# Kernel tuning notes

Hardware: AMD Instinct MI355X
Metric: run time of the kernel (lower is better)

The kernel has to match this reference:

```python
import jax, jax.numpy as jnp
import numpy as np

P, B, A, NT = 2, 96, 32, 24
N = B * A
MD, MA, MW = 4, 4, 2
NPOLB = MD + MA
C_LK = 0.089793561062583294  # 1 / (2 * pi**1.5)


def _norm(v):
    return v / jnp.sqrt(jnp.sum(v * v, -1, keepdims=True) + 1e-12)


def _gat_atoms(c, i):
    # c: [P,B,A,3], i: [P,B,K] -> [P,B,K,3]
    return jnp.take_along_axis(c, jnp.broadcast_to(i[..., None], i.shape + (3,)), axis=2)


def setup_inputs():
    key = jax.random.key(0)
    rng = np.random.default_rng(0)
    inp = {}
    inp["pose_coords"] = jax.random.normal(key, (P, N, 3), jnp.float32) * 8.0
    inp["pose_stack_block_type"] = jnp.asarray(rng.integers(0, NT, (P, B)), jnp.int32)
    inp["pose_stack_min_bond_separation"] = jnp.full((P, B, B), 6, jnp.int32)
    inp["bt_n_atoms"] = jnp.full((NT,), A, jnp.int32)
    bonds = np.stack([np.arange(A), (np.arange(A) + 1) % A], -1)
    inp["bt_all_bonds"] = jnp.asarray(np.broadcast_to(bonds, (NT, A, 2)).copy(), jnp.int32)
    rngs = np.stack([np.arange(A), np.arange(A) + 1], -1)
    inp["bt_atom_all_bond_ranges"] = jnp.asarray(np.broadcast_to(rngs, (NT, A, 2)).copy(), jnp.int32)
    inp["bt_tile_n_donH"] = jnp.asarray(rng.integers(1, MD + 1, (NT,)), jnp.int32)
    inp["bt_tile_n_acc"] = jnp.asarray(rng.integers(1, MA + 1, (NT,)), jnp.int32)
    donH = np.broadcast_to(2 * np.arange(MD) + 1, (NT, MD)).copy()
    inp["bt_tile_donH_inds"] = jnp.asarray(donH, jnp.int32)
    inp["bt_tile_don_hvy_inds"] = jnp.asarray(donH - 1, jnp.int32)
    inp["bt_tile_acc_inds"] = jnp.asarray(np.broadcast_to(8 + np.arange(MA), (NT, MA)).copy(), jnp.int32)
    inp["bt_tile_hybridization"] = jnp.asarray(rng.integers(0, 3, (NT, MA)), jnp.int32)
    is_h = np.zeros((NT, A), np.int32)
    is_h[:, 1:8:2] = 1
    inp["bt_atom_is_hydrogen"] = jnp.asarray(is_h)
    par = np.empty((NT, A, 4), np.float32)
    par[..., 0] = rng.uniform(1.4, 2.2, (NT, A))   # lj_radius
    par[..., 1] = rng.uniform(-6.0, 6.0, (NT, A))  # lk_dgfree
    par[..., 2] = rng.uniform(3.0, 3.6, (NT, A))   # lk_lambda
    par[..., 3] = rng.uniform(3.0, 15.0, (NT, A))  # lk_volume
    inp["bt_tile_lk_ball_params"] = jnp.asarray(par)
    pd = np.minimum(np.abs(np.arange(A)[:, None] - np.arange(A)[None, :]), 6)
    inp["bt_path_distance"] = jnp.asarray(np.broadcast_to(pd, (NT, A, A)).copy(), jnp.int32)
    inp["lk_ball_global_params"] = jnp.asarray([6.0, 3.709, 2.828], jnp.float32)   # cutoff, ramp_width_A2, d2_low
    inp["water_gen_global_params"] = jnp.asarray([2.65, 2.0943951], jnp.float32)   # water dist, water bond angle
    inp["sp2_water_tors"] = jnp.asarray([0.0, np.pi], jnp.float32)
    inp["sp3_water_tors"] = jnp.asarray([np.pi / 3.0, -np.pi / 3.0], jnp.float32)
    inp["ring_water_tors"] = jnp.asarray([0.0, np.pi / 2.0], jnp.float32)
    return inp


def reference(pose_coords, pose_stack_block_type, pose_stack_min_bond_separation,
              bt_n_atoms, bt_all_bonds, bt_atom_all_bond_ranges,
              bt_tile_n_donH, bt_tile_n_acc, bt_tile_donH_inds, bt_tile_don_hvy_inds,
              bt_tile_acc_inds, bt_tile_hybridization, bt_atom_is_hydrogen,
              bt_tile_lk_ball_params, bt_path_distance,
              lk_ball_global_params, water_gen_global_params,
              sp2_water_tors, sp3_water_tors, ring_water_tors):
    bt = pose_stack_block_type
    coords = pose_coords.reshape(P, B, A, 3)
    wdist = water_gen_global_params[0]
    wang = water_gen_global_params[1]
    # ---- step 1a: donor waters placed along heavy->H direction ----
    hvy_i = bt_tile_don_hvy_inds[bt]
    H_i = bt_tile_donH_inds[bt]                                              # [P,B,MD]
    hvy = _gat_atoms(coords, hvy_i)
    Hxyz = _gat_atoms(coords, H_i)
    don_w = hvy + wdist * _norm(Hxyz - hvy)                                  # [P,B,MD,3]
    don_mask = jnp.arange(MD) < bt_tile_n_donH[bt][..., None]                # [P,B,MD]
    don_w = jnp.broadcast_to(don_w[..., None, :], (P, B, MD, MW, 3))
    don_wm = don_mask[..., None] & (jnp.arange(MW) == 0)                     # one water per donH
    # ---- step 1b: acceptor waters via hybridization-dependent torsion (NeRF) ----
    acc_i = bt_tile_acc_inds[bt]                                             # [P,B,MA]
    ranges0 = bt_atom_all_bond_ranges[bt][..., 0]                            # [P,B,A]
    bonds1 = bt_all_bonds[bt][..., 1]                                        # [P,B,A]
    base_i = jnp.take_along_axis(bonds1, jnp.take_along_axis(ranges0, acc_i, axis=2), axis=2)
    base2_i = jnp.take_along_axis(bonds1, jnp.take_along_axis(ranges0, base_i, axis=2), axis=2)
    cxyz = _gat_atoms(coords, acc_i)
    bxyz = _gat_atoms(coords, base_i)
    axyz = _gat_atoms(coords, base2_i)
    e1 = _norm(cxyz - bxyz)
    nrm = _norm(jnp.cross(bxyz - axyz, e1))
    e2 = jnp.cross(nrm, e1)
    tors_tab = jnp.stack([sp2_water_tors, sp3_water_tors, ring_water_tors])  # [3,MW]
    chi = tors_tab[bt_tile_hybridization[bt]]                                # [P,B,MA,MW]
    ct, st = jnp.cos(wang), jnp.sin(wang)
    acc_w = (cxyz[..., None, :]
             + (-wdist * ct) * e1[..., None, :]
             + (wdist * st) * jnp.cos(chi)[..., None] * e2[..., None, :]
             + (wdist * st) * jnp.sin(chi)[..., None] * nrm[..., None, :])   # [P,B,MA,MW,3]
    acc_mask = jnp.arange(MA) < bt_tile_n_acc[bt][..., None]
    acc_wm = jnp.broadcast_to(acc_mask[..., None], (P, B, MA, MW))
    # ---- assemble polar sites + waters ----
    waters = jnp.concatenate([don_w, acc_w], axis=2).reshape(P, B * NPOLB, MW, 3)
    wmask = jnp.concatenate([don_wm, acc_wm], axis=2).reshape(P, B * NPOLB, MW)
    pol_loc = jnp.concatenate([hvy_i, acc_i], axis=2)                        # [P,B,NPOLB]
    pol_mask = jnp.concatenate([don_mask, acc_mask], axis=2).reshape(P, B * NPOLB)
    gidx = (jnp.arange(B)[None, :, None] * A + pol_loc).reshape(P, B * NPOLB)
    # ---- gather per-atom data ----
    params_flat = bt_tile_lk_ball_params[bt].reshape(P, N, 4)
    heavy = bt_atom_is_hydrogen[bt].reshape(P, N) == 0
    xp = jnp.take_along_axis(pose_coords, jnp.broadcast_to(gidx[..., None], gidx.shape + (3,)), axis=1)
    pp = jnp.take_along_axis(params_flat, jnp.broadcast_to(gidx[..., None], gidx.shape + (4,)), axis=1)
    # ---- step 2: pair distances + bond-separation mask ----
    diff = xp[:, :, None, :] - pose_coords[:, None, :, :]                    # [P,NPOL,N,3]
    d2 = jnp.maximum(jnp.sum(diff * diff, -1), 1e-2)
    d = jnp.sqrt(d2)
    b_i = gidx // A
    a_i = gidx % A
    b_j = jnp.arange(N) // A
    a_j = jnp.arange(N) % A
    bti = jnp.take_along_axis(bt, b_i, axis=1)
    intra = bt_path_distance[bti[:, :, None], a_i[:, :, None], a_j[None, None, :]]
    inter = pose_stack_min_bond_separation[jnp.arange(P)[:, None, None], b_i[:, :, None], b_j[None, None, :]]
    sep = jnp.where(b_i[:, :, None] == b_j[None, None, :], intra, inter)
    cutoff = lk_ball_global_params[0]
    ramp2 = lk_ball_global_params[1]
    d2_low = lk_ball_global_params[2]
    mask = (sep >= 4) & heavy[:, None, :] & pol_mask[:, :, None] & (d < cutoff)
    # ---- isotropic LK desolvation of polar atom i by occluder j ----
    ri, dgi, lami = pp[..., 0], pp[..., 1], pp[..., 2]
    rj, volj = params_flat[..., 0], params_flat[..., 3]
    x = (d - (ri[:, :, None] + rj[:, None, :])) / lami[:, :, None]
    lk_iso = C_LK * dgi[:, :, None] * volj[:, None, :] / lami[:, :, None] * jnp.exp(-x * x) / d2
    lk_iso = jnp.where(mask, lk_iso, 0.0)
    # ---- lk-ball fraction from water-site occlusion ----
    wdiff = waters[:, :, :, None, :] - pose_coords[:, None, None, :, :]      # [P,NPOL,MW,N,3]
    d2w = jnp.sum(wdiff * wdiff, -1)
    d2w = jnp.where(wmask[..., None], d2w, 1e9)
    d2wmin = jnp.min(d2w, axis=2)                                            # [P,NPOL,N]
    wt = jnp.clip((d2_low + ramp2 - d2wmin) / ramp2, 0.0, 1.0)
    frac = wt * wt * (3.0 - 2.0 * wt)
    return jnp.stack([jnp.sum(lk_iso, (1, 2)), jnp.sum(lk_iso * frac, (1, 2))])  # [2,P]
```

## Files before the change

### kernel.cpp

```cpp
#include <hip/hip_runtime.h>
#include <math.h>

constexpr int P  = 2;
constexpr int B  = 96;
constexpr int A  = 32;
constexpr int N  = B * A;
constexpr int MD = 4;
constexpr int MA = 4;
constexpr int NPOL = MD + MA;
constexpr int SJ = 2;
constexpr int JS = N / SJ;
constexpr int JPT = JS / 256;
constexpr float C_LK = 0.0897935610625833f;

__global__ void zero_out_kernel(float* out) {
    int t = threadIdx.x;
    if (t < 2 * P) out[t] = 0.0f;
}

__global__ __launch_bounds__(256) void lkball_kernel(
    const float* __restrict__ pose_coords,
    const int*   __restrict__ block_type,
    const int*   __restrict__ min_sep,
    const int*   __restrict__ all_bonds,
    const int*   __restrict__ bond_ranges,
    const int*   __restrict__ n_donH,
    const int*   __restrict__ n_acc,
    const int*   __restrict__ donH_inds,
    const int*   __restrict__ don_hvy_inds,
    const int*   __restrict__ acc_inds,
    const int*   __restrict__ hyb,
    const int*   __restrict__ is_h,
    const float* __restrict__ lk_params,
    const int*   __restrict__ path_dist,
    const float* __restrict__ glob,
    const float* __restrict__ wglob,
    const float* __restrict__ sp2t,
    const float* __restrict__ sp3t,
    const float* __restrict__ ringt,
    float*       __restrict__ out)
{
    __shared__ float spolar[NPOL][16];
    __shared__ int   spolai[NPOL];
    __shared__ int   s_bt[B];
    __shared__ int   smsep[B];
    __shared__ int   spath[NPOL * A];
    __shared__ float red0[4], red1[4];

    const int bid   = blockIdx.x;
    const int p     = bid / (B * SJ);
    const int rem   = bid % (B * SJ);
    const int b     = rem / SJ;
    const int slice = rem % SJ;
    const int tid   = threadIdx.x;

    if (tid < NPOL) {
        const int k  = tid;
        const int bt = block_type[p * B + b];
        const float wdist = wglob[0];
        const float wang  = wglob[1];
        float xp[3], w0[3], w1[3];
        int   a_i, valid;
        if (k < MD) {
            valid = (k < n_donH[bt]) ? 1 : 0;
            const int hvy = don_hvy_inds[bt * MD + k];
            const int Hi  = donH_inds[bt * MD + k];
            a_i = hvy;
            const float* hc = pose_coords + (size_t)(p * N + b * A + hvy) * 3;
            const float* Hc = pose_coords + (size_t)(p * N + b * A + Hi) * 3;
            float dx = Hc[0] - hc[0], dy = Hc[1] - hc[1], dz = Hc[2] - hc[2];
            float inv = 1.0f / sqrtf(dx * dx + dy * dy + dz * dz + 1e-12f);
            xp[0] = hc[0]; xp[1] = hc[1]; xp[2] = hc[2];
            w0[0] = hc[0] + wdist * dx * inv;
            w0[1] = hc[1] + wdist * dy * inv;
            w0[2] = hc[2] + wdist * dz * inv;
            w1[0] = hc[0] + 1.0e3f; w1[1] = hc[1] + 1.0e3f; w1[2] = hc[2] + 1.0e3f;
        } else {
            const int kk = k - MD;
            valid = (kk < n_acc[bt]) ? 1 : 0;
            const int ai = acc_inds[bt * MA + kk];
            a_i = ai;
            const int r0    = bond_ranges[(bt * A + ai) * 2 + 0];
            const int base  = all_bonds[(bt * A + r0) * 2 + 1];
            const int r0b   = bond_ranges[(bt * A + base) * 2 + 0];
            const int base2 = all_bonds[(bt * A + r0b) * 2 + 1];
            const float* c  = pose_coords + (size_t)(p * N + b * A + ai)    * 3;
            const float* bx = pose_coords + (size_t)(p * N + b * A + base)  * 3;
            const float* ax = pose_coords + (size_t)(p * N + b * A + base2) * 3;

            float e1x = c[0] - bx[0], e1y = c[1] - bx[1], e1z = c[2] - bx[2];
            float inv1 = 1.0f / sqrtf(e1x * e1x + e1y * e1y + e1z * e1z + 1e-12f);
            e1x *= inv1; e1y *= inv1; e1z *= inv1;

            float ux = bx[0] - ax[0], uy = bx[1] - ax[1], uz = bx[2] - ax[2];
            float nx = uy * e1z - uz * e1y;
            float ny = uz * e1x - ux * e1z;
            float nz = ux * e1y - uy * e1x;
            float inv2 = 1.0f / sqrtf(nx * nx + ny * ny + nz * nz + 1e-12f);
            nx *= inv2; ny *= inv2; nz *= inv2;
            float e2x = ny * e1z - nz * e1y;
            float e2y = nz * e1x - nx * e1z;
            float e2z = nx * e1y - ny * e1x;

            const int hy = hyb[bt * MA + kk];
            const float* tab = (hy == 0) ? sp2t : ((hy == 1) ? sp3t : ringt);
            const float ct = cosf(wang), st = sinf(wang);
            float c0 = cosf(tab[0]), s0 = sinf(tab[0]);
            float c1 = cosf(tab[1]), s1 = sinf(tab[1]);

            xp[0] = c[0]; xp[1] = c[1]; xp[2] = c[2];
            w0[0] = c[0] - wdist * ct * e1x + wdist * st * c0 * e2x + wdist * st * s0 * nx;
            w0[1] = c[1] - wdist * ct * e1y + wdist * st * c0 * e2y + wdist * st * s0 * ny;
            w0[2] = c[2] - wdist * ct * e1z + wdist * st * c0 * e2z + wdist * st * s0 * nz;
            w1[0] = c[0] - wdist * ct * e1x + wdist * st * c1 * e2x + wdist * st * s1 * nx;
            w1[1] = c[1] - wdist * ct * e1y + wdist * st * c1 * e2y + wdist * st * s1 * ny;
            w1[2] = c[2] - wdist * ct * e1z + wdist * st * c1 * e2z + wdist * st * s1 * nz;
        }
        const float* pr = lk_params + (size_t)(bt * A + a_i) * 4;
        const float lam = pr[2];
        spolar[k][0] = xp[0]; spolar[k][1] = xp[1]; spolar[k][2] = xp[2];
        spolar[k][3] = w0[0]; spolar[k][4] = w0[1]; spolar[k][5] = w0[2];
        spolar[k][6] = w1[0]; spolar[k][7] = w1[1]; spolar[k][8] = w1[2];
        spolar[k][9]  = pr[0];
        spolar[k][10] = valid ? (C_LK * pr[1] / lam) : 0.0f;
        spolar[k][11] = 1.0f / lam;
        spolai[k] = a_i;
    }
    if (tid >= 64 && tid < 64 + B)   s_bt[tid - 64]   = block_type[p * B + (tid - 64)];
    if (tid >= 160 && tid < 160 + B) smsep[tid - 160] = min_sep[(p * B + b) * B + (tid - 160)];
    __syncthreads();

    {
        const int k  = tid >> 5;
        const int aj = tid & 31;
        const int bt = s_bt[b];
        spath[tid] = path_dist[(bt * A + spolai[k]) * A + aj];
    }
    __syncthreads();

    const float cutoff = glob[0];
    const float inv_ramp2 = 1.0f / glob[1];
    const float c3 = glob[2] + glob[1];
    const int a_j = tid & 31;
    const int jbase = slice * JS + tid;

    float cx[JPT], cy[JPT], cz[JPT], rj[JPT], ve[JPT];
    float msep_f[JPT];
    int   intra[JPT];
#pragma unroll
    for (int i = 0; i < JPT; ++i) {
        const int j   = jbase + 256 * i;
        const int b_j = j >> 5;
        const float* cj = pose_coords + (size_t)(p * N + j) * 3;
        cx[i] = cj[0]; cy[i] = cj[1]; cz[i] = cj[2];
        const int bt_j = s_bt[b_j];
        const int hv   = is_h[bt_j * A + a_j];
        const float4 pj = *(const float4*)(lk_params + (size_t)(bt_j * A + a_j) * 4);
        rj[i] = pj.x;
        ve[i] = hv ? 0.0f : pj.w;
        msep_f[i] = (float)smsep[b_j];
        intra[i]  = (b_j == b);
    }

    float acc0 = 0.0f, acc1 = 0.0f;

#pragma unroll
    for (int k = 0; k < NPOL; ++k) {
        const float px = spolar[k][0], py = spolar[k][1], pz = spolar[k][2];
        const float w0x = spolar[k][3], w0y = spolar[k][4], w0z = spolar[k][5];
        const float w1x = spolar[k][6], w1y = spolar[k][7], w1z = spolar[k][8];
        const float ri = spolar[k][9], pref = spolar[k][10], inv_lam = spolar[k][11];
        const float path_k = (float)spath[k * A + a_j];

#pragma unroll
        for (int i = 0; i < JPT; ++i) {
            const float dx = px - cx[i], dy = py - cy[i], dz = pz - cz[i];
            float d2 = fmaf(dx, dx, fmaf(dy, dy, dz * dz));
            d2 = fmaxf(d2, 0.01f);
            const float d = __builtin_amdgcn_sqrtf(d2);
            const float sep = intra[i] ? path_k : msep_f[i];
            const bool ok = (sep >= 4.0f) & (d < cutoff);

            const float x = (d - ri - rj[i]) * inv_lam;
            float lk = pref * ve[i] * __expf(-x * x) * __builtin_amdgcn_rcpf(d2);
            lk = ok ? lk : 0.0f;

            const float d0x = w0x - cx[i], d0y = w0y - cy[i], d0z = w0z - cz[i];
            const float d1x = w1x - cx[i], d1y = w1y - cy[i], d1z = w1z - cz[i];
            const float d2w0 = fmaf(d0x, d0x, fmaf(d0y, d0y, d0z * d0z));
            const float d2w1 = fmaf(d1x, d1x, fmaf(d1y, d1y, d1z * d1z));
            const float d2wmin = fminf(d2w0, d2w1);
            float wt = (c3 - d2wmin) * inv_ramp2;
            wt = fminf(fmaxf(wt, 0.0f), 1.0f);
            const float frac = wt * wt * (3.0f - 2.0f * wt);

            acc0 += lk;
            acc1 = fmaf(lk, frac, acc1);
        }
    }

    for (int off = 32; off > 0; off >>= 1) {
        acc0 += __shfl_down(acc0, off);
        acc1 += __shfl_down(acc1, off);
    }
    const int wave = tid >> 6;
    const int lane = tid & 63;
    if (lane == 0) { red0[wave] = acc0; red1[wave] = acc1; }
    __syncthreads();
    if (tid == 0) {
        atomicAdd(&out[p],     red0[0] + red0[1] + red0[2] + red0[3]);
        atomicAdd(&out[P + p], red1[0] + red1[1] + red1[2] + red1[3]);
    }
}

extern "C" void kernel_launch(void* const* d_in, const int* in_sizes, int n_in,
                              void* d_out, int out_size, void* d_ws, size_t ws_size,
                              hipStream_t stream) {
    const float* pose_coords  = (const float*)d_in[0];
    const int*   block_type   = (const int*)  d_in[1];
    const int*   min_sep      = (const int*)  d_in[2];
    const int*   all_bonds    = (const int*)  d_in[4];
    const int*   bond_ranges  = (const int*)  d_in[5];
    const int*   n_donH       = (const int*)  d_in[6];
    const int*   n_acc        = (const int*)  d_in[7];
    const int*   donH_inds    = (const int*)  d_in[8];
    const int*   don_hvy_inds = (const int*)  d_in[9];
    const int*   acc_inds     = (const int*)  d_in[10];
    const int*   hyb          = (const int*)  d_in[11];
    const int*   is_h         = (const int*)  d_in[12];
    const float* lk_params    = (const float*)d_in[13];
    const int*   path_dist    = (const int*)  d_in[14];
    const float* glob         = (const float*)d_in[15];
    const float* wglob        = (const float*)d_in[16];
    const float* sp2t         = (const float*)d_in[17];
    const float* sp3t         = (const float*)d_in[18];
    const float* ringt        = (const float*)d_in[19];
    float* out = (float*)d_out;

    zero_out_kernel<<<1, 64, 0, stream>>>(out);

    const int nblocks = P * B * SJ;
    lkball_kernel<<<nblocks, 256, 0, stream>>>(
        pose_coords, block_type, min_sep, all_bonds, bond_ranges,
        n_donH, n_acc, donH_inds, don_hvy_inds, acc_inds, hyb, is_h,
        lk_params, path_dist, glob, wglob, sp2t, sp3t, ringt, out);
}
```

Measured before the change: 113.1 us.

## Precompute polar-atom water sites in a prep kernel and split occluders finer

```diff
diff --git a/kernel.cpp b/kernel.cpp
--- a/kernel.cpp
+++ b/kernel.cpp
@@ -8,20 +8,17 @@
 constexpr int MD = 4;
 constexpr int MA = 4;
 constexpr int NPOL = MD + MA;
-constexpr int SJ = 2;
+constexpr int SJ = 4;
 constexpr int JS = N / SJ;
 constexpr int JPT = JS / 256;
-constexpr float C_LK = 0.0897935610625833f;
-
-__global__ void zero_out_kernel(float* out) {
-    int t = threadIdx.x;
-    if (t < 2 * P) out[t] = 0.0f;
-}
-
-__global__ __launch_bounds__(256) void lkball_kernel(
+constexpr int NPTOT = P * B * NPOL;
+constexpr float C_LK  = 0.0897935610625833f;
+constexpr float LOG2E = 1.4426950408889634f;
+
+
+__global__ __launch_bounds__(256) void prep_kernel(
     const float* __restrict__ pose_coords,
     const int*   __restrict__ block_type,
-    const int*   __restrict__ min_sep,
     const int*   __restrict__ all_bonds,
     const int*   __restrict__ bond_ranges,
     const int*   __restrict__ n_donH,
@@ -30,18 +27,108 @@
     const int*   __restrict__ don_hvy_inds,
     const int*   __restrict__ acc_inds,
     const int*   __restrict__ hyb,
+    const float* __restrict__ lk_params,
+    const float* __restrict__ wglob,
+    const float* __restrict__ sp2t,
+    const float* __restrict__ sp3t,
+    const float* __restrict__ ringt,
+    float*       __restrict__ ws,
+    float*       __restrict__ out)
+{
+    const int t = blockIdx.x * 256 + threadIdx.x;
+    if (t < 2 * P) out[t] = 0.0f;
+    if (t >= NPTOT) return;
+
+    const int p = t / (B * NPOL);
+    const int r = t % (B * NPOL);
+    const int b = r / NPOL;
+    const int k = r % NPOL;
+    const int bt = block_type[p * B + b];
+    const float wdist = wglob[0];
+    const float wang  = wglob[1];
+
+    float xp[3], w0[3], w1[3];
+    int a_i, valid;
+    if (k < MD) {
+        valid = (k < n_donH[bt]) ? 1 : 0;
+        const int hvy = don_hvy_inds[bt * MD + k];
+        const int Hi  = donH_inds[bt * MD + k];
+        a_i = hvy;
+        const float* hc = pose_coords + (size_t)(p * N + b * A + hvy) * 3;
+        const float* Hc = pose_coords + (size_t)(p * N + b * A + Hi) * 3;
+        float dx = Hc[0] - hc[0], dy = Hc[1] - hc[1], dz = Hc[2] - hc[2];
+        float inv = 1.0f / sqrtf(dx * dx + dy * dy + dz * dz + 1e-12f);
+        xp[0] = hc[0]; xp[1] = hc[1]; xp[2] = hc[2];
+        w0[0] = hc[0] + wdist * dx * inv;
+        w0[1] = hc[1] + wdist * dy * inv;
+        w0[2] = hc[2] + wdist * dz * inv;
+        w1[0] = hc[0] + 1.0e3f; w1[1] = hc[1] + 1.0e3f; w1[2] = hc[2] + 1.0e3f;
+    } else {
+        const int kk = k - MD;
+        valid = (kk < n_acc[bt]) ? 1 : 0;
+        const int ai = acc_inds[bt * MA + kk];
+        a_i = ai;
+        const int r0    = bond_ranges[(bt * A + ai) * 2 + 0];
+        const int base  = all_bonds[(bt * A + r0) * 2 + 1];
+        const int r0b   = bond_ranges[(bt * A + base) * 2 + 0];
+        const int base2 = all_bonds[(bt * A + r0b) * 2 + 1];
+        const float* c  = pose_coords + (size_t)(p * N + b * A + ai)    * 3;
+        const float* bx = pose_coords + (size_t)(p * N + b * A + base)  * 3;
+        const float* ax = pose_coords + (size_t)(p * N + b * A + base2) * 3;
+
+        float e1x = c[0] - bx[0], e1y = c[1] - bx[1], e1z = c[2] - bx[2];
+        float inv1 = 1.0f / sqrtf(e1x * e1x + e1y * e1y + e1z * e1z + 1e-12f);
+        e1x *= inv1; e1y *= inv1; e1z *= inv1;
+
+        float ux = bx[0] - ax[0], uy = bx[1] - ax[1], uz = bx[2] - ax[2];
+        float nx = uy * e1z - uz * e1y;
+        float ny = uz * e1x - ux * e1z;
+        float nz = ux * e1y - uy * e1x;
+        float inv2 = 1.0f / sqrtf(nx * nx + ny * ny + nz * nz + 1e-12f);
+        nx *= inv2; ny *= inv2; nz *= inv2;
+        float e2x = ny * e1z - nz * e1y;
+        float e2y = nz * e1x - nx * e1z;
+        float e2z = nx * e1y - ny * e1x;
+
+        const int hy = hyb[bt * MA + kk];
+        const float* tab = (hy == 0) ? sp2t : ((hy == 1) ? sp3t : ringt);
+        const float ct = cosf(wang), st = sinf(wang);
+        float c0 = cosf(tab[0]), s0 = sinf(tab[0]);
+        float c1 = cosf(tab[1]), s1 = sinf(tab[1]);
+
+        xp[0] = c[0]; xp[1] = c[1]; xp[2] = c[2];
+        w0[0] = c[0] - wdist * ct * e1x + wdist * st * c0 * e2x + wdist * st * s0 * nx;
+        w0[1] = c[1] - wdist * ct * e1y + wdist * st * c0 * e2y + wdist * st * s0 * ny;
+        w0[2] = c[2] - wdist * ct * e1z + wdist * st * c0 * e2z + wdist * st * s0 * nz;
+        w1[0] = c[0] - wdist * ct * e1x + wdist * st * c1 * e2x + wdist * st * s1 * nx;
+        w1[1] = c[1] - wdist * ct * e1y + wdist * st * c1 * e2y + wdist * st * s1 * ny;
+        w1[2] = c[2] - wdist * ct * e1z + wdist * st * c1 * e2z + wdist * st * s1 * nz;
+    }
+    const float* pr = lk_params + (size_t)(bt * A + a_i) * 4;
+    const float lam = pr[2];
+    float* dst = ws + (size_t)t * 16;
+    dst[0]  = xp[0]; dst[1] = xp[1]; dst[2] = xp[2];
+    dst[3]  = w0[0]; dst[4] = w0[1]; dst[5] = w0[2];
+    dst[6]  = w1[0]; dst[7] = w1[1]; dst[8] = w1[2];
+    dst[9]  = pr[0];
+    dst[10] = valid ? (C_LK * pr[1] / lam) : 0.0f;
+    dst[11] = -LOG2E / (lam * lam);
+    dst[12] = __int_as_float(a_i);
+    dst[13] = 0.0f; dst[14] = 0.0f; dst[15] = 0.0f;
+}
+
+__global__ __launch_bounds__(256, 3) void lkball_kernel(
+    const float* __restrict__ pose_coords,
+    const int*   __restrict__ block_type,
+    const int*   __restrict__ min_sep,
     const int*   __restrict__ is_h,
     const float* __restrict__ lk_params,
     const int*   __restrict__ path_dist,
     const float* __restrict__ glob,
-    const float* __restrict__ wglob,
-    const float* __restrict__ sp2t,
-    const float* __restrict__ sp3t,
-    const float* __restrict__ ringt,
+    const float* __restrict__ ws,
     float*       __restrict__ out)
 {
     __shared__ float spolar[NPOL][16];
-    __shared__ int   spolai[NPOL];
     __shared__ int   s_bt[B];
     __shared__ int   smsep[B];
     __shared__ int   spath[NPOL * A];
@@ -54,77 +141,9 @@
     const int slice = rem % SJ;
     const int tid   = threadIdx.x;
 
-    if (tid < NPOL) {
-        const int k  = tid;
-        const int bt = block_type[p * B + b];
-        const float wdist = wglob[0];
-        const float wang  = wglob[1];
-        float xp[3], w0[3], w1[3];
-        int   a_i, valid;
-        if (k < MD) {
-            valid = (k < n_donH[bt]) ? 1 : 0;
-            const int hvy = don_hvy_inds[bt * MD + k];
-            const int Hi  = donH_inds[bt * MD + k];
-            a_i = hvy;
-            const float* hc = pose_coords + (size_t)(p * N + b * A + hvy) * 3;
-            const float* Hc = pose_coords + (size_t)(p * N + b * A + Hi) * 3;
-            float dx = Hc[0] - hc[0], dy = Hc[1] - hc[1], dz = Hc[2] - hc[2];
-            float inv = 1.0f / sqrtf(dx * dx + dy * dy + dz * dz + 1e-12f);
-            xp[0] = hc[0]; xp[1] = hc[1]; xp[2] = hc[2];
-            w0[0] = hc[0] + wdist * dx * inv;
-            w0[1] = hc[1] + wdist * dy * inv;
-            w0[2] = hc[2] + wdist * dz * inv;
-            w1[0] = hc[0] + 1.0e3f; w1[1] = hc[1] + 1.0e3f; w1[2] = hc[2] + 1.0e3f;
-        } else {
-            const int kk = k - MD;
-            valid = (kk < n_acc[bt]) ? 1 : 0;
-            const int ai = acc_inds[bt * MA + kk];
-            a_i = ai;
-            const int r0    = bond_ranges[(bt * A + ai) * 2 + 0];
-            const int base  = all_bonds[(bt * A + r0) * 2 + 1];
-            const int r0b   = bond_ranges[(bt * A + base) * 2 + 0];
-            const int base2 = all_bonds[(bt * A + r0b) * 2 + 1];
-            const float* c  = pose_coords + (size_t)(p * N + b * A + ai)    * 3;
-            const float* bx = pose_coords + (size_t)(p * N + b * A + base)  * 3;
-            const float* ax = pose_coords + (size_t)(p * N + b * A + base2) * 3;
-
-            float e1x = c[0] - bx[0], e1y = c[1] - bx[1], e1z = c[2] - bx[2];
-            float inv1 = 1.0f / sqrtf(e1x * e1x + e1y * e1y + e1z * e1z + 1e-12f);
-            e1x *= inv1; e1y *= inv1; e1z *= inv1;
-
-            float ux = bx[0] - ax[0], uy = bx[1] - ax[1], uz = bx[2] - ax[2];
-            float nx = uy * e1z - uz * e1y;
-            float ny = uz * e1x - ux * e1z;
-            float nz = ux * e1y - uy * e1x;
-            float inv2 = 1.0f / sqrtf(nx * nx + ny * ny + nz * nz + 1e-12f);
-            nx *= inv2; ny *= inv2; nz *= inv2;
-            float e2x = ny * e1z - nz * e1y;
-            float e2y = nz * e1x - nx * e1z;
-            float e2z = nx * e1y - ny * e1x;
-
-            const int hy = hyb[bt * MA + kk];
-            const float* tab = (hy == 0) ? sp2t : ((hy == 1) ? sp3t : ringt);
-            const float ct = cosf(wang), st = sinf(wang);
-            float c0 = cosf(tab[0]), s0 = sinf(tab[0]);
-            float c1 = cosf(tab[1]), s1 = sinf(tab[1]);
-
-            xp[0] = c[0]; xp[1] = c[1]; xp[2] = c[2];
-            w0[0] = c[0] - wdist * ct * e1x + wdist * st * c0 * e2x + wdist * st * s0 * nx;
-            w0[1] = c[1] - wdist * ct * e1y + wdist * st * c0 * e2y + wdist * st * s0 * ny;
-            w0[2] = c[2] - wdist * ct * e1z + wdist * st * c0 * e2z + wdist * st * s0 * nz;
-            w1[0] = c[0] - wdist * ct * e1x + wdist * st * c1 * e2x + wdist * st * s1 * nx;
-            w1[1] = c[1] - wdist * ct * e1y + wdist * st * c1 * e2y + wdist * st * s1 * ny;
-            w1[2] = c[2] - wdist * ct * e1z + wdist * st * c1 * e2z + wdist * st * s1 * nz;
-        }
-        const float* pr = lk_params + (size_t)(bt * A + a_i) * 4;
-        const float lam = pr[2];
-        spolar[k][0] = xp[0]; spolar[k][1] = xp[1]; spolar[k][2] = xp[2];
-        spolar[k][3] = w0[0]; spolar[k][4] = w0[1]; spolar[k][5] = w0[2];
-        spolar[k][6] = w1[0]; spolar[k][7] = w1[1]; spolar[k][8] = w1[2];
-        spolar[k][9]  = pr[0];
-        spolar[k][10] = valid ? (C_LK * pr[1] / lam) : 0.0f;
-        spolar[k][11] = 1.0f / lam;
-        spolai[k] = a_i;
+    if (tid < 32) {
+        const float4* src = (const float4*)(ws + (size_t)((p * B + b) * NPOL) * 16);
+        ((float4*)spolar)[tid] = src[tid];
     }
     if (tid >= 64 && tid < 64 + B)   s_bt[tid - 64]   = block_type[p * B + (tid - 64)];
     if (tid >= 160 && tid < 160 + B) smsep[tid - 160] = min_sep[(p * B + b) * B + (tid - 160)];
@@ -134,18 +153,18 @@
         const int k  = tid >> 5;
         const int aj = tid & 31;
         const int bt = s_bt[b];
-        spath[tid] = path_dist[(bt * A + spolai[k]) * A + aj];
+        const int ak = __float_as_int(spolar[k][12]);
+        spath[tid] = path_dist[(bt * A + ak) * A + aj];
     }
     __syncthreads();
 
-    const float cutoff = glob[0];
+    const float cutoff    = glob[0];
     const float inv_ramp2 = 1.0f / glob[1];
-    const float c3 = glob[2] + glob[1];
-    const int a_j = tid & 31;
+    const float c4        = (glob[2] + glob[1]) * inv_ramp2;
+    const int a_j   = tid & 31;
     const int jbase = slice * JS + tid;
 
-    float cx[JPT], cy[JPT], cz[JPT], rj[JPT], ve[JPT];
-    float msep_f[JPT];
+    float cx[JPT], cy[JPT], cz[JPT], rj[JPT], ve[JPT], msep_f[JPT];
     int   intra[JPT];
 #pragma unroll
     for (int i = 0; i < JPT; ++i) {
@@ -166,10 +185,13 @@
 
 #pragma unroll
     for (int k = 0; k < NPOL; ++k) {
-        const float px = spolar[k][0], py = spolar[k][1], pz = spolar[k][2];
-        const float w0x = spolar[k][3], w0y = spolar[k][4], w0z = spolar[k][5];
-        const float w1x = spolar[k][6], w1y = spolar[k][7], w1z = spolar[k][8];
-        const float ri = spolar[k][9], pref = spolar[k][10], inv_lam = spolar[k][11];
+        const float4 q0 = ((const float4*)spolar[k])[0];
+        const float4 q1 = ((const float4*)spolar[k])[1];
+        const float4 q2 = ((const float4*)spolar[k])[2];
+        const float px  = q0.x, py  = q0.y, pz  = q0.z;
+        const float w0x = q0.w, w0y = q1.x, w0z = q1.y;
+        const float w1x = q1.z, w1y = q1.w, w1z = q2.x;
+        const float ri  = q2.y, pref = q2.z, negq = q2.w;
         const float path_k = (float)spath[k * A + a_j];
 
 #pragma unroll
@@ -177,12 +199,14 @@
             const float dx = px - cx[i], dy = py - cy[i], dz = pz - cz[i];
             float d2 = fmaf(dx, dx, fmaf(dy, dy, dz * dz));
             d2 = fmaxf(d2, 0.01f);
-            const float d = __builtin_amdgcn_sqrtf(d2);
+            const float rinv = __builtin_amdgcn_rsqf(d2);
+            const float d = d2 * rinv;
             const float sep = intra[i] ? path_k : msep_f[i];
             const bool ok = (sep >= 4.0f) & (d < cutoff);
 
-            const float x = (d - ri - rj[i]) * inv_lam;
-            float lk = pref * ve[i] * __expf(-x * x) * __builtin_amdgcn_rcpf(d2);
+            const float t = d - ri - rj[i];
+            const float e = __builtin_amdgcn_exp2f(t * t * negq);
+            float lk = pref * ve[i] * e * (rinv * rinv);
             lk = ok ? lk : 0.0f;
 
             const float d0x = w0x - cx[i], d0y = w0y - cy[i], d0z = w0z - cz[i];
@@ -190,9 +214,9 @@
             const float d2w0 = fmaf(d0x, d0x, fmaf(d0y, d0y, d0z * d0z));
             const float d2w1 = fmaf(d1x, d1x, fmaf(d1y, d1y, d1z * d1z));
             const float d2wmin = fminf(d2w0, d2w1);
-            float wt = (c3 - d2wmin) * inv_ramp2;
+            float wt = fmaf(d2wmin, -inv_ramp2, c4);
             wt = fminf(fmaxf(wt, 0.0f), 1.0f);
-            const float frac = wt * wt * (3.0f - 2.0f * wt);
+            const float frac = wt * wt * fmaf(-2.0f, wt, 3.0f);
 
             acc0 += lk;
             acc1 = fmaf(lk, frac, acc1);
@@ -236,12 +260,15 @@
     const float* sp3t         = (const float*)d_in[18];
     const float* ringt        = (const float*)d_in[19];
     float* out = (float*)d_out;
-
-    zero_out_kernel<<<1, 64, 0, stream>>>(out);
+    float* ws  = (float*)d_ws;
+
+    prep_kernel<<<NPTOT / 256, 256, 0, stream>>>(
+        pose_coords, block_type, all_bonds, bond_ranges,
+        n_donH, n_acc, donH_inds, don_hvy_inds, acc_inds, hyb,
+        lk_params, wglob, sp2t, sp3t, ringt, ws, out);
 
     const int nblocks = P * B * SJ;
     lkball_kernel<<<nblocks, 256, 0, stream>>>(
-        pose_coords, block_type, min_sep, all_bonds, bond_ranges,
-        n_donH, n_acc, donH_inds, don_hvy_inds, acc_inds, hyb, is_h,
-        lk_params, path_dist, glob, wglob, sp2t, sp3t, ringt, out);
+        pose_coords, block_type, min_sep, is_h,
+        lk_params, path_dist, glob, ws, out);
 }
```

Result: slower. 122.2 us (+8.0%).
